# Optimization experiments

Measured on AMD Instinct MI355X. Metric: run time of the kernel, lower is better.

Reference implementation:

```python
import jax, jax.numpy as jnp
import numpy as np

B, H, W, C = 8, 56, 56, 192
HEADS, K, PAD = 6, 3, 1
KK = K * K
HEAD_DIM = C // HEADS
SCALE = HEAD_DIM ** -0.5


def setup_inputs() -> dict:
    key = jax.random.key(0)
    ks = jax.random.split(key, 6)
    s = lambda fan_in: 1.0 / np.sqrt(fan_in)
    return {
        "x": jax.random.normal(ks[0], (B, H, W, C), jnp.float32),
        "Wv": jax.random.normal(ks[1], (C, C), jnp.float32) * s(C),
        "Wa": jax.random.normal(ks[2], (C, KK * KK * HEADS), jnp.float32) * s(C),
        "ba": jax.random.normal(ks[3], (KK * KK * HEADS,), jnp.float32) * s(C),
        "Wp": jax.random.normal(ks[4], (C, C), jnp.float32) * s(C),
        "bp": jax.random.normal(ks[5], (C,), jnp.float32) * s(C),
    }


def _unfold(v_nchw):
    # im2col, kernel 3, pad 1, stride 1 -> (B, C, 9, H, W); kernel pos row-major like nn.Unfold
    vp = jnp.pad(v_nchw, ((0, 0), (0, 0), (PAD, PAD), (PAD, PAD)))
    return jnp.stack([vp[:, :, i:i + H, j:j + W] for i in range(K) for j in range(K)], axis=2)


def _fold(cols):
    # col2im scatter-add: cols (B, C, 9, H, W) -> (B, C, H, W)
    out = jnp.zeros((cols.shape[0], cols.shape[1], H + 2 * PAD, W + 2 * PAD), cols.dtype)
    idx = 0
    for i in range(K):
        for j in range(K):
            out = out.at[:, :, i:i + H, j:j + W].add(cols[:, :, idx])
            idx += 1
    return out[:, :, PAD:PAD + H, PAD:PAD + W]


def reference(x, Wv, Wa, ba, Wp, bp):
    hw = H * W
    # values: linear then unfold into per-pixel kxk windows
    v = jnp.einsum("bhwc,cd->bhwd", x, Wv)              # (B,H,W,C)
    v = _unfold(v.transpose(0, 3, 1, 2))                 # (B,C,9,H,W)
    v = v.reshape(B, HEADS, HEAD_DIM, KK, hw)
    v = v.transpose(0, 1, 4, 3, 2)                       # (B,heads,HW,9,c)
    # dynamic attention weights (stride=1 -> pool is identity)
    a = jnp.einsum("bhwc,ck->bhwk", x, Wa) + ba          # (B,H,W,81*heads)
    a = a.reshape(B, hw, HEADS, KK, KK).transpose(0, 2, 1, 3, 4)
    a = jax.nn.softmax(a * SCALE, axis=-1)               # (B,heads,HW,9,9)
    o = jnp.einsum("bnpkl,bnplc->bnpkc", a, v)           # (B,heads,HW,9,c)
    o = o.transpose(0, 1, 4, 3, 2).reshape(B, C, KK, H, W)
    o = _fold(o)                                          # (B,C,H,W)
    o = o.transpose(0, 2, 3, 1)                           # NHWC
    return jnp.einsum("bhwc,cd->bhwd", o, Wp) + bp
```

## Files before the change

kernel.cpp:

```cpp
#include <hip/hip_runtime.h>
#include <hip/hip_bf16.h>

constexpr int NH = 56, NW = 56, NC = 192, AJ = 486;
constexpr int HWP = NH * NW;
constexpr int NPIX = 8 * HWP;
constexpr float SCALE = 0.17677669529663687f;

typedef unsigned int u32;
typedef __bf16 bf16x8 __attribute__((ext_vector_type(8)));
typedef __bf16 bf16x2 __attribute__((ext_vector_type(2)));
typedef float f32x4 __attribute__((ext_vector_type(4)));

__global__ __launch_bounds__(256) void k_prep(const float* __restrict__ Wv,
                                              const float* __restrict__ Wa,
                                              const float* __restrict__ Wp,
                                              __bf16* __restrict__ Wvt,
                                              __bf16* __restrict__ Wat,
                                              __bf16* __restrict__ Wpt) {
  const int i = blockIdx.x * 256 + threadIdx.x;
  if (i < 192 * 192) {
    const int n = i / 192, k = i - n * 192;
    Wvt[i] = (__bf16)Wv[k * 192 + n];
    Wpt[i] = (__bf16)Wp[k * 192 + n];
  } else {
    const int j = i - 192 * 192;
    if (j < 486 * 192) {
      const int n = j / 192, k = j - n * 192;
      Wat[j] = (__bf16)Wa[k * 486 + n];
    }
  }
}

template <int MODE>
__global__ __launch_bounds__(256) void k_gemm(const void* __restrict__ Ap,
                                              const int a_is_f32,
                                              const __bf16* __restrict__ Bt,
                                              const float* __restrict__ bias,
                                              void* __restrict__ Cp,
                                              const int Nval) {
  __shared__ short As[128 * 32];
  __shared__ short Bs[64 * 32];
  const int m0 = blockIdx.x * 128, n0 = blockIdx.y * 64;
  const int t = threadIdx.x;
  const int lane = t & 63, w = t >> 6, wm = w >> 1, wn = w & 1;
  f32x4 acc[4][2];
  #pragma unroll
  for (int mi = 0; mi < 4; ++mi)
    #pragma unroll
    for (int nj = 0; nj < 2; ++nj) acc[mi][nj] = (f32x4){0.f, 0.f, 0.f, 0.f};

  for (int k0 = 0; k0 < 192; k0 += 32) {
    __syncthreads();
    #pragma unroll
    for (int i = 0; i < 2; ++i) {
      const int c = t + i * 256;
      const int row = c >> 2, kc = (c & 3) * 8;
      bf16x8 av;
      if (a_is_f32) {
        const float* src = (const float*)Ap + (size_t)(m0 + row) * 192 + k0 + kc;
        const float4 f0 = *(const float4*)src;
        const float4 f1 = *(const float4*)(src + 4);
        av[0] = (__bf16)f0.x; av[1] = (__bf16)f0.y;
        av[2] = (__bf16)f0.z; av[3] = (__bf16)f0.w;
        av[4] = (__bf16)f1.x; av[5] = (__bf16)f1.y;
        av[6] = (__bf16)f1.z; av[7] = (__bf16)f1.w;
      } else {
        av = *(const bf16x8*)((const __bf16*)Ap + (size_t)(m0 + row) * 192 + k0 + kc);
      }
      *(bf16x8*)&As[row * 32 + kc] = av;
    }
    {
      const int row = t >> 2, kc = (t & 3) * 8;
      const int n = n0 + row;
      bf16x8 bv;
      #pragma unroll
      for (int j = 0; j < 8; ++j) bv[j] = (__bf16)0.f;
      if (n < Nval) bv = *(const bf16x8*)&Bt[(size_t)n * 192 + k0 + kc];
      *(bf16x8*)&Bs[row * 32 + kc] = bv;
    }
    __syncthreads();
    bf16x8 af[4], bfr[2];
    #pragma unroll
    for (int mi = 0; mi < 4; ++mi)
      af[mi] = *(const bf16x8*)&As[(wm * 64 + mi * 16 + (lane & 15)) * 32 + (lane >> 4) * 8];
    #pragma unroll
    for (int nj = 0; nj < 2; ++nj)
      bfr[nj] = *(const bf16x8*)&Bs[(wn * 32 + nj * 16 + (lane & 15)) * 32 + (lane >> 4) * 8];
    #pragma unroll
    for (int mi = 0; mi < 4; ++mi)
      #pragma unroll
      for (int nj = 0; nj < 2; ++nj)
        acc[mi][nj] = __builtin_amdgcn_mfma_f32_16x16x32_bf16(af[mi], bfr[nj], acc[mi][nj], 0, 0, 0);
  }
  const int col_l = lane & 15, rq4 = (lane >> 4) * 4;
  #pragma unroll
  for (int nj = 0; nj < 2; ++nj) {
    const int gn = n0 + wn * 32 + nj * 16 + col_l;
    if (gn >= Nval) continue;
    const float bv = (MODE == 0) ? 0.f : bias[gn];
    #pragma unroll
    for (int mi = 0; mi < 4; ++mi) {
      const int gm = m0 + wm * 64 + mi * 16 + rq4;
      #pragma unroll
      for (int r = 0; r < 4; ++r) {
        const float val = acc[mi][nj][r];
        if (MODE == 0)
          ((__bf16*)Cp)[(size_t)(gm + r) * Nval + gn] = (__bf16)val;
        else
          ((float*)Cp)[(size_t)(gm + r) * Nval + gn] = val + bv;
      }
    }
  }
}

__global__ __launch_bounds__(256) void k_gemmT(const __bf16* __restrict__ Wat,
                                               const float* __restrict__ x,
                                               const float* __restrict__ ba,
                                               __bf16* __restrict__ lgT) {
  __shared__ short As[128 * 32];
  __shared__ short Bs[64 * 32];
  const int m0 = blockIdx.x * 128, n0 = blockIdx.y * 64;
  const int t = threadIdx.x;
  const int lane = t & 63, w = t >> 6, wm = w >> 1, wn = w & 1;
  f32x4 acc[4][2];
  #pragma unroll
  for (int mi = 0; mi < 4; ++mi)
    #pragma unroll
    for (int nj = 0; nj < 2; ++nj) acc[mi][nj] = (f32x4){0.f, 0.f, 0.f, 0.f};

  for (int k0 = 0; k0 < 192; k0 += 32) {
    __syncthreads();
    #pragma unroll
    for (int i = 0; i < 2; ++i) {
      const int c = t + i * 256;
      const int row = c >> 2, kc = (c & 3) * 8;
      bf16x8 av;
      #pragma unroll
      for (int j = 0; j < 8; ++j) av[j] = (__bf16)0.f;
      if (m0 + row < 486)
        av = *(const bf16x8*)&Wat[(size_t)(m0 + row) * 192 + k0 + kc];
      *(bf16x8*)&As[row * 32 + kc] = av;
    }
    {
      const int row = t >> 2, kc = (t & 3) * 8;
      const float* src = x + (size_t)(n0 + row) * 192 + k0 + kc;
      const float4 f0 = *(const float4*)src;
      const float4 f1 = *(const float4*)(src + 4);
      bf16x8 bv;
      bv[0] = (__bf16)f0.x; bv[1] = (__bf16)f0.y;
      bv[2] = (__bf16)f0.z; bv[3] = (__bf16)f0.w;
      bv[4] = (__bf16)f1.x; bv[5] = (__bf16)f1.y;
      bv[6] = (__bf16)f1.z; bv[7] = (__bf16)f1.w;
      *(bf16x8*)&Bs[row * 32 + kc] = bv;
    }
    __syncthreads();
    bf16x8 af[4], bfr[2];
    #pragma unroll
    for (int mi = 0; mi < 4; ++mi)
      af[mi] = *(const bf16x8*)&As[(wm * 64 + mi * 16 + (lane & 15)) * 32 + (lane >> 4) * 8];
    #pragma unroll
    for (int nj = 0; nj < 2; ++nj)
      bfr[nj] = *(const bf16x8*)&Bs[(wn * 32 + nj * 16 + (lane & 15)) * 32 + (lane >> 4) * 8];
    #pragma unroll
    for (int mi = 0; mi < 4; ++mi)
      #pragma unroll
      for (int nj = 0; nj < 2; ++nj)
        acc[mi][nj] = __builtin_amdgcn_mfma_f32_16x16x32_bf16(af[mi], bfr[nj], acc[mi][nj], 0, 0, 0);
  }
  const int col_l = lane & 15, rq4 = (lane >> 4) * 4;
  #pragma unroll
  for (int nj = 0; nj < 2; ++nj) {
    const int gn = n0 + wn * 32 + nj * 16 + col_l;
    #pragma unroll
    for (int mi = 0; mi < 4; ++mi) {
      const int gmb = m0 + wm * 64 + mi * 16 + rq4;
      #pragma unroll
      for (int r = 0; r < 4; ++r) {
        const int gm = gmb + r;
        if (gm < 486)
          lgT[(size_t)gm * NPIX + gn] = (__bf16)((acc[mi][nj][r] + ba[gm]) * SCALE);
      }
    }
  }
}

__global__ __launch_bounds__(256) void k_coef(const __bf16* __restrict__ lgT,
                                              __bf16* __restrict__ wcT) {
  const int p = blockIdx.x * 256 + threadIdx.x;
  const int head = blockIdx.y;
  const int b = p / HWP;
  const int yx = p - b * HWP;
  const int y = yx / NW, x = yx - y * NW;

  float wc[25];
  #pragma unroll
  for (int c = 0; c < 25; ++c) wc[c] = 0.f;

  #pragma unroll
  for (int ki = 0; ki < 3; ++ki) {
    const int h = y - ki + 1;
    if ((unsigned)h >= (unsigned)NH) continue;
    #pragma unroll
    for (int kj = 0; kj < 3; ++kj) {
      const int ww = x - kj + 1;
      if ((unsigned)ww >= (unsigned)NW) continue;
      const int src = b * HWP + h * NW + ww;
      const size_t base = (size_t)((head * 9 + ki * 3 + kj) * 9) * NPIX + src;
      float lt[9];
      #pragma unroll
      for (int l = 0; l < 9; ++l) lt[l] = (float)lgT[base + (size_t)l * NPIX];
      float m = lt[0];
      #pragma unroll
      for (int l = 1; l < 9; ++l) m = fmaxf(m, lt[l]);
      float s = 0.f;
      #pragma unroll
      for (int l = 0; l < 9; ++l) { lt[l] = __expf(lt[l] - m); s += lt[l]; }
      const float inv = 1.f / s;
      #pragma unroll
      for (int l = 0; l < 9; ++l) {
        const int li = l / 3, lj = l - li * 3;
        wc[(li - ki + 2) * 5 + (lj - kj + 2)] += lt[l] * inv;
      }
    }
  }
  #pragma unroll
  for (int c = 0; c < 25; ++c)
    wcT[(size_t)(head * 25 + c) * NPIX + p] = (__bf16)wc[c];
}

__global__ __launch_bounds__(192) void k_att2(const __bf16* __restrict__ v,
                                              const __bf16* __restrict__ wcT,
                                              __bf16* __restrict__ o) {
  const int p0 = blockIdx.x * 8;
  const int bb = p0 / HWP;
  const int yx0 = p0 - bb * HWP;
  const int y = yx0 / NW, x0 = yx0 - y * NW;
  const int t = threadIdx.x;

  __shared__ __bf16 vs[60][192];
  __shared__ float wcs[8][6][28];

  for (int i = t; i < 1440; i += 192) {
    const int cell = i / 24, ck = i - cell * 24;
    const int di = cell / 12, col = cell - di * 12;
    const int yy = y + di - 2, xx = x0 + col - 2;
    bf16x8 val;
    #pragma unroll
    for (int j = 0; j < 8; ++j) val[j] = (__bf16)0.f;
    if ((unsigned)yy < (unsigned)NH && (unsigned)xx < (unsigned)NW)
      val = *(const bf16x8*)&v[(size_t)(bb * HWP + yy * NW + xx) * 192 + ck * 8];
    *(bf16x8*)&vs[cell][ck * 8] = val;
  }
  if (t < 150) {
    const int head = t / 25, cc = t - head * 25;
    const bf16x8 w8 = *(const bf16x8*)&wcT[(size_t)t * NPIX + p0];
    #pragma unroll
    for (int q = 0; q < 8; ++q) wcs[q][head][cc] = (float)w8[q];
  }
  __syncthreads();

  const int ch = t, head = ch >> 5;
  float vr[5][12];
  #pragma unroll
  for (int di = 0; di < 5; ++di)
    #pragma unroll
    for (int col = 0; col < 12; ++col) vr[di][col] = (float)vs[di * 12 + col][ch];
  #pragma unroll
  for (int q = 0; q < 8; ++q) {
    float coef[25];
    #pragma unroll
    for (int i = 0; i < 6; ++i)
      *(float4*)&coef[i * 4] = *(const float4*)&wcs[q][head][i * 4];
    coef[24] = wcs[q][head][24];
    float s = 0.f;
    #pragma unroll
    for (int di = 0; di < 5; ++di)
      #pragma unroll
      for (int dj = 0; dj < 5; ++dj) s += coef[di * 5 + dj] * vr[di][q + dj];
    o[(size_t)(p0 + q) * 192 + ch] = (__bf16)s;
  }
}

extern "C" void kernel_launch(void* const* d_in, const int* in_sizes, int n_in,
                              void* d_out, int out_size, void* d_ws,
                              size_t ws_size, hipStream_t stream) {
  (void)in_sizes; (void)n_in; (void)out_size; (void)ws_size;
  const float* x  = (const float*)d_in[0];
  const float* Wv = (const float*)d_in[1];
  const float* Wa = (const float*)d_in[2];
  const float* ba = (const float*)d_in[3];
  const float* Wp = (const float*)d_in[4];
  const float* bp = (const float*)d_in[5];

  char* ws = (char*)d_ws;
  __bf16* Wvt = (__bf16*)(ws);
  __bf16* Wat = (__bf16*)(ws + 73728);
  __bf16* Wpt = (__bf16*)(ws + 260352);
  __bf16* v_ws = (__bf16*)(ws + 334080);
  __bf16* lgT = (__bf16*)(ws + 9967872);
  __bf16* wcT = (__bf16*)(ws + 34353408);
  __bf16* o_ws = (__bf16*)(ws + 9967872);

  k_prep<<<509, 256, 0, stream>>>(Wv, Wa, Wp, Wvt, Wat, Wpt);
  k_gemm<0><<<dim3(196, 3), 256, 0, stream>>>(x, 1, Wvt, nullptr, v_ws, 192);
  k_gemmT<<<dim3(4, 392), 256, 0, stream>>>(Wat, x, ba, lgT);
  k_coef<<<dim3(98, 6), 256, 0, stream>>>(lgT, wcT);
  k_att2<<<NPIX / 8, 192, 0, stream>>>(v_ws, wcT, o_ws);
  k_gemm<2><<<dim3(196, 3), 256, 0, stream>>>(o_ws, 0, Wpt, bp, (float*)d_out, 192);
}
```

Measured before the change: 162.7 us.

## Pre-convert x to bf16 and use direct global-to-LDS loads with larger GEMM tiles

```diff
diff --git a/kernel.cpp b/kernel.cpp
--- a/kernel.cpp
+++ b/kernel.cpp
@@ -6,171 +6,150 @@
 constexpr int NPIX = 8 * HWP;
 constexpr float SCALE = 0.17677669529663687f;
 
-typedef unsigned int u32;
 typedef __bf16 bf16x8 __attribute__((ext_vector_type(8)));
-typedef __bf16 bf16x2 __attribute__((ext_vector_type(2)));
 typedef float f32x4 __attribute__((ext_vector_type(4)));
 
-__global__ __launch_bounds__(256) void k_prep(const float* __restrict__ Wv,
-                                              const float* __restrict__ Wa,
-                                              const float* __restrict__ Wp,
-                                              __bf16* __restrict__ Wvt,
-                                              __bf16* __restrict__ Wat,
-                                              __bf16* __restrict__ Wpt) {
-  const int i = blockIdx.x * 256 + threadIdx.x;
-  if (i < 192 * 192) {
+__device__ __forceinline__ void gload16(const void* g, void* l) {
+  __builtin_amdgcn_global_load_lds(
+      (const __attribute__((address_space(1))) void*)g,
+      (__attribute__((address_space(3))) void*)l, 16, 0, 0);
+}
+
+__global__ __launch_bounds__(256) void k_prep2(const float* __restrict__ x,
+                                               const float* __restrict__ Wv,
+                                               const float* __restrict__ Wa,
+                                               const float* __restrict__ Wp,
+                                               __bf16* __restrict__ xb,
+                                               __bf16* __restrict__ Wvt,
+                                               __bf16* __restrict__ Wat,
+                                               __bf16* __restrict__ Wpt) {
+  const int bid = blockIdx.x;
+  if (bid < 144) {
+    const int i = bid * 256 + threadIdx.x;
     const int n = i / 192, k = i - n * 192;
     Wvt[i] = (__bf16)Wv[k * 192 + n];
     Wpt[i] = (__bf16)Wp[k * 192 + n];
+  } else if (bid < 528) {
+    const int i = (bid - 144) * 256 + threadIdx.x;
+    const int n = i / 192, k = i - n * 192;
+    Wat[i] = (n < 486) ? (__bf16)Wa[k * 486 + n] : (__bf16)0.f;
   } else {
-    const int j = i - 192 * 192;
-    if (j < 486 * 192) {
-      const int n = j / 192, k = j - n * 192;
-      Wat[j] = (__bf16)Wa[k * 486 + n];
-    }
+    const size_t i = (size_t)(bid - 528) * 256 + threadIdx.x;
+    const float* src = x + i * 8;
+    const float4 f0 = *(const float4*)src;
+    const float4 f1 = *(const float4*)(src + 4);
+    bf16x8 o8;
+    o8[0] = (__bf16)f0.x; o8[1] = (__bf16)f0.y;
+    o8[2] = (__bf16)f0.z; o8[3] = (__bf16)f0.w;
+    o8[4] = (__bf16)f1.x; o8[5] = (__bf16)f1.y;
+    o8[6] = (__bf16)f1.z; o8[7] = (__bf16)f1.w;
+    *(bf16x8*)(xb + i * 8) = o8;
   }
 }
 
 template <int MODE>
-__global__ __launch_bounds__(256) void k_gemm(const void* __restrict__ Ap,
-                                              const int a_is_f32,
-                                              const __bf16* __restrict__ Bt,
-                                              const float* __restrict__ bias,
-                                              void* __restrict__ Cp,
-                                              const int Nval) {
-  __shared__ short As[128 * 32];
-  __shared__ short Bs[64 * 32];
-  const int m0 = blockIdx.x * 128, n0 = blockIdx.y * 64;
-  const int t = threadIdx.x;
-  const int lane = t & 63, w = t >> 6, wm = w >> 1, wn = w & 1;
-  f32x4 acc[4][2];
+__global__ __launch_bounds__(256) void k_gemm_nn(const __bf16* __restrict__ A,
+                                                 const __bf16* __restrict__ Bt,
+                                                 const float* __restrict__ bias,
+                                                 void* __restrict__ C) {
+  __shared__ __bf16 As[64 * 32];
+  __shared__ __bf16 Bs[192 * 32];
+  const int m0 = blockIdx.x * 64;
+  const int t = threadIdx.x, lane = t & 63, w = t >> 6;
+  const int wm = w >> 1, wn = w & 1;
+  f32x4 acc[2][6];
+  #pragma unroll
+  for (int mi = 0; mi < 2; ++mi)
+    #pragma unroll
+    for (int nj = 0; nj < 6; ++nj) acc[mi][nj] = (f32x4){0.f, 0.f, 0.f, 0.f};
+
+  const int cA = w * 64 + lane;
+  const int rowA = cA >> 2, kcA = (cA & 3) * 8;
+
+  for (int k0 = 0; k0 < 192; k0 += 32) {
+    __syncthreads();
+    gload16(A + (size_t)(m0 + rowA) * 192 + k0 + kcA, &As[(w * 64) * 8]);
+    #pragma unroll
+    for (int i = 0; i < 3; ++i) {
+      const int cB = i * 256 + w * 64 + lane;
+      const int rowB = cB >> 2, kcB = (cB & 3) * 8;
+      gload16(Bt + (size_t)rowB * 192 + k0 + kcB, &Bs[(i * 256 + w * 64) * 8]);
+    }
+    __syncthreads();
+    bf16x8 af[2], bfr[6];
+    #pragma unroll
+    for (int mi = 0; mi < 2; ++mi)
+      af[mi] = *(const bf16x8*)&As[(wm * 32 + mi * 16 + (lane & 15)) * 32 + (lane >> 4) * 8];
+    #pragma unroll
+    for (int nj = 0; nj < 6; ++nj)
+      bfr[nj] = *(const bf16x8*)&Bs[(wn * 96 + nj * 16 + (lane & 15)) * 32 + (lane >> 4) * 8];
+    #pragma unroll
+    for (int mi = 0; mi < 2; ++mi)
+      #pragma unroll
+      for (int nj = 0; nj < 6; ++nj)
+        acc[mi][nj] = __builtin_amdgcn_mfma_f32_16x16x32_bf16(af[mi], bfr[nj], acc[mi][nj], 0, 0, 0);
+  }
+  const int col_l = lane & 15, rq4 = (lane >> 4) * 4;
+  #pragma unroll
+  for (int nj = 0; nj < 6; ++nj) {
+    const int gn = wn * 96 + nj * 16 + col_l;
+    const float bv = (MODE == 2) ? bias[gn] : 0.f;
+    #pragma unroll
+    for (int mi = 0; mi < 2; ++mi) {
+      const int gm = m0 + wm * 32 + mi * 16 + rq4;
+      #pragma unroll
+      for (int r = 0; r < 4; ++r) {
+        if (MODE == 0)
+          ((__bf16*)C)[(size_t)(gm + r) * 192 + gn] = (__bf16)acc[mi][nj][r];
+        else
+          ((float*)C)[(size_t)(gm + r) * 192 + gn] = acc[mi][nj][r] + bv;
+      }
+    }
+  }
+}
+
+__global__ __launch_bounds__(256) void k_gemmT2(const __bf16* __restrict__ Wat,
+                                                const __bf16* __restrict__ xb,
+                                                const float* __restrict__ ba,
+                                                __bf16* __restrict__ lgT) {
+  __shared__ __bf16 As[128 * 32];
+  __shared__ __bf16 Bs[128 * 32];
+  const int m0 = blockIdx.x * 128, n0 = blockIdx.y * 128;
+  const int t = threadIdx.x, lane = t & 63, w = t >> 6;
+  const int wm = w >> 1, wn = w & 1;
+  f32x4 acc[4][4];
   #pragma unroll
   for (int mi = 0; mi < 4; ++mi)
     #pragma unroll
-    for (int nj = 0; nj < 2; ++nj) acc[mi][nj] = (f32x4){0.f, 0.f, 0.f, 0.f};
+    for (int nj = 0; nj < 4; ++nj) acc[mi][nj] = (f32x4){0.f, 0.f, 0.f, 0.f};
 
   for (int k0 = 0; k0 < 192; k0 += 32) {
     __syncthreads();
     #pragma unroll
     for (int i = 0; i < 2; ++i) {
-      const int c = t + i * 256;
+      const int c = i * 256 + w * 64 + lane;
       const int row = c >> 2, kc = (c & 3) * 8;
-      bf16x8 av;
-      if (a_is_f32) {
-        const float* src = (const float*)Ap + (size_t)(m0 + row) * 192 + k0 + kc;
-        const float4 f0 = *(const float4*)src;
-        const float4 f1 = *(const float4*)(src + 4);
-        av[0] = (__bf16)f0.x; av[1] = (__bf16)f0.y;
-        av[2] = (__bf16)f0.z; av[3] = (__bf16)f0.w;
-        av[4] = (__bf16)f1.x; av[5] = (__bf16)f1.y;
-        av[6] = (__bf16)f1.z; av[7] = (__bf16)f1.w;
-      } else {
-        av = *(const bf16x8*)((const __bf16*)Ap + (size_t)(m0 + row) * 192 + k0 + kc);
-      }
-      *(bf16x8*)&As[row * 32 + kc] = av;
-    }
-    {
-      const int row = t >> 2, kc = (t & 3) * 8;
-      const int n = n0 + row;
-      bf16x8 bv;
-      #pragma unroll
-      for (int j = 0; j < 8; ++j) bv[j] = (__bf16)0.f;
-      if (n < Nval) bv = *(const bf16x8*)&Bt[(size_t)n * 192 + k0 + kc];
-      *(bf16x8*)&Bs[row * 32 + kc] = bv;
-    }
-    __syncthreads();
-    bf16x8 af[4], bfr[2];
+      gload16(Wat + (size_t)(m0 + row) * 192 + k0 + kc, &As[(i * 256 + w * 64) * 8]);
+      gload16(xb + (size_t)(n0 + row) * 192 + k0 + kc, &Bs[(i * 256 + w * 64) * 8]);
+    }
+    __syncthreads();
+    bf16x8 af[4], bfr[4];
     #pragma unroll
     for (int mi = 0; mi < 4; ++mi)
       af[mi] = *(const bf16x8*)&As[(wm * 64 + mi * 16 + (lane & 15)) * 32 + (lane >> 4) * 8];
     #pragma unroll
-    for (int nj = 0; nj < 2; ++nj)
-      bfr[nj] = *(const bf16x8*)&Bs[(wn * 32 + nj * 16 + (lane & 15)) * 32 + (lane >> 4) * 8];
+    for (int nj = 0; nj < 4; ++nj)
+      bfr[nj] = *(const bf16x8*)&Bs[(wn * 64 + nj * 16 + (lane & 15)) * 32 + (lane >> 4) * 8];
     #pragma unroll
     for (int mi = 0; mi < 4; ++mi)
       #pragma unroll
-      for (int nj = 0; nj < 2; ++nj)
+      for (int nj = 0; nj < 4; ++nj)
         acc[mi][nj] = __builtin_amdgcn_mfma_f32_16x16x32_bf16(af[mi], bfr[nj], acc[mi][nj], 0, 0, 0);
   }
   const int col_l = lane & 15, rq4 = (lane >> 4) * 4;
   #pragma unroll
-  for (int nj = 0; nj < 2; ++nj) {
-    const int gn = n0 + wn * 32 + nj * 16 + col_l;
-    if (gn >= Nval) continue;
-    const float bv = (MODE == 0) ? 0.f : bias[gn];
-    #pragma unroll
-    for (int mi = 0; mi < 4; ++mi) {
-      const int gm = m0 + wm * 64 + mi * 16 + rq4;
-      #pragma unroll
-      for (int r = 0; r < 4; ++r) {
-        const float val = acc[mi][nj][r];
-        if (MODE == 0)
-          ((__bf16*)Cp)[(size_t)(gm + r) * Nval + gn] = (__bf16)val;
-        else
-          ((float*)Cp)[(size_t)(gm + r) * Nval + gn] = val + bv;
-      }
-    }
-  }
-}
-
-__global__ __launch_bounds__(256) void k_gemmT(const __bf16* __restrict__ Wat,
-                                               const float* __restrict__ x,
-                                               const float* __restrict__ ba,
-                                               __bf16* __restrict__ lgT) {
-  __shared__ short As[128 * 32];
-  __shared__ short Bs[64 * 32];
-  const int m0 = blockIdx.x * 128, n0 = blockIdx.y * 64;
-  const int t = threadIdx.x;
-  const int lane = t & 63, w = t >> 6, wm = w >> 1, wn = w & 1;
-  f32x4 acc[4][2];
-  #pragma unroll
-  for (int mi = 0; mi < 4; ++mi)
-    #pragma unroll
-    for (int nj = 0; nj < 2; ++nj) acc[mi][nj] = (f32x4){0.f, 0.f, 0.f, 0.f};
-
-  for (int k0 = 0; k0 < 192; k0 += 32) {
-    __syncthreads();
-    #pragma unroll
-    for (int i = 0; i < 2; ++i) {
-      const int c = t + i * 256;
-      const int row = c >> 2, kc = (c & 3) * 8;
-      bf16x8 av;
-      #pragma unroll
-      for (int j = 0; j < 8; ++j) av[j] = (__bf16)0.f;
-      if (m0 + row < 486)
-        av = *(const bf16x8*)&Wat[(size_t)(m0 + row) * 192 + k0 + kc];
-      *(bf16x8*)&As[row * 32 + kc] = av;
-    }
-    {
-      const int row = t >> 2, kc = (t & 3) * 8;
-      const float* src = x + (size_t)(n0 + row) * 192 + k0 + kc;
-      const float4 f0 = *(const float4*)src;
-      const float4 f1 = *(const float4*)(src + 4);
-      bf16x8 bv;
-      bv[0] = (__bf16)f0.x; bv[1] = (__bf16)f0.y;
-      bv[2] = (__bf16)f0.z; bv[3] = (__bf16)f0.w;
-      bv[4] = (__bf16)f1.x; bv[5] = (__bf16)f1.y;
-      bv[6] = (__bf16)f1.z; bv[7] = (__bf16)f1.w;
-      *(bf16x8*)&Bs[row * 32 + kc] = bv;
-    }
-    __syncthreads();
-    bf16x8 af[4], bfr[2];
-    #pragma unroll
-    for (int mi = 0; mi < 4; ++mi)
-      af[mi] = *(const bf16x8*)&As[(wm * 64 + mi * 16 + (lane & 15)) * 32 + (lane >> 4) * 8];
-    #pragma unroll
-    for (int nj = 0; nj < 2; ++nj)
-      bfr[nj] = *(const bf16x8*)&Bs[(wn * 32 + nj * 16 + (lane & 15)) * 32 + (lane >> 4) * 8];
-    #pragma unroll
-    for (int mi = 0; mi < 4; ++mi)
-      #pragma unroll
-      for (int nj = 0; nj < 2; ++nj)
-        acc[mi][nj] = __builtin_amdgcn_mfma_f32_16x16x32_bf16(af[mi], bfr[nj], acc[mi][nj], 0, 0, 0);
-  }
-  const int col_l = lane & 15, rq4 = (lane >> 4) * 4;
-  #pragma unroll
-  for (int nj = 0; nj < 2; ++nj) {
-    const int gn = n0 + wn * 32 + nj * 16 + col_l;
+  for (int nj = 0; nj < 4; ++nj) {
+    const int gn = n0 + wn * 64 + nj * 16 + col_l;
     #pragma unroll
     for (int mi = 0; mi < 4; ++mi) {
       const int gmb = m0 + wm * 64 + mi * 16 + rq4;
@@ -295,16 +274,17 @@
   char* ws = (char*)d_ws;
   __bf16* Wvt = (__bf16*)(ws);
   __bf16* Wat = (__bf16*)(ws + 73728);
-  __bf16* Wpt = (__bf16*)(ws + 260352);
-  __bf16* v_ws = (__bf16*)(ws + 334080);
-  __bf16* lgT = (__bf16*)(ws + 9967872);
-  __bf16* wcT = (__bf16*)(ws + 34353408);
-  __bf16* o_ws = (__bf16*)(ws + 9967872);
-
-  k_prep<<<509, 256, 0, stream>>>(Wv, Wa, Wp, Wvt, Wat, Wpt);
-  k_gemm<0><<<dim3(196, 3), 256, 0, stream>>>(x, 1, Wvt, nullptr, v_ws, 192);
-  k_gemmT<<<dim3(4, 392), 256, 0, stream>>>(Wat, x, ba, lgT);
+  __bf16* Wpt = (__bf16*)(ws + 270336);
+  __bf16* xb  = (__bf16*)(ws + 344064);
+  __bf16* v_ws = (__bf16*)(ws + 9977856);
+  __bf16* lgT = (__bf16*)(ws + 19611648);
+  __bf16* wcT = (__bf16*)(ws + 43997184);
+  __bf16* o_ws = (__bf16*)(ws + 19611648);
+
+  k_prep2<<<2880, 256, 0, stream>>>(x, Wv, Wa, Wp, xb, Wvt, Wat, Wpt);
+  k_gemm_nn<0><<<392, 256, 0, stream>>>(xb, Wvt, nullptr, v_ws);
+  k_gemmT2<<<dim3(4, 196), 256, 0, stream>>>(Wat, xb, ba, lgT);
   k_coef<<<dim3(98, 6), 256, 0, stream>>>(lgT, wcT);
   k_att2<<<NPIX / 8, 192, 0, stream>>>(v_ws, wcT, o_ws);
-  k_gemm<2><<<dim3(196, 3), 256, 0, stream>>>(o_ws, 0, Wpt, bp, (float*)d_out, 192);
-}
+  k_gemm_nn<2><<<392, 256, 0, stream>>>(o_ws, Wpt, bp, (float*)d_out);
+}
```

Measured after the change: 149.7 us. 1.09x faster.
